# Kernel optimization log

Measured on AMD Instinct MI355X. Metric: run time of the kernel, lower is better.

Reference implementation:

```python
import jax, jax.numpy as jnp
import numpy as np

V, D, H = 50000, 256, 4
HD = H * D            # concat head dim (TransformerConv concat=True)
HH, O = 256, 256      # invariant_hidden_dim, invariant_out_dim
B, N, E, L, A = 16, 1000, 4000, 64, 128
PAD = 0
SCALE = 1.0 / float(np.sqrt(D))


def emb_lookup(table, idx):
    # nn.Embedding with padding_idx: forward is a plain gather; grad at pad row is zeroed.
    rows = table[idx]
    return jnp.where((idx == PAD)[..., None], jax.lax.stop_gradient(rows), rows)


def transformer_conv(x, edge_index, ea, Wq, bq, Wk, bk, Wv, bv, We, Wskip, bskip):
    # PyG TransformerConv, heads=H, concat=True, root_weight=True, beta=False, dropout=0 (eval)
    n = x.shape[0]
    src, dst = edge_index[0], edge_index[1]
    q = (x @ Wq + bq).reshape(n, H, D)
    e = (ea @ We).reshape(-1, H, D)          # lin_edge (bias=False)
    k = (x @ Wk + bk).reshape(n, H, D)[src] + e
    v = (x @ Wv + bv).reshape(n, H, D)[src] + e
    alpha = (q[dst] * k).sum(-1) * SCALE      # [E,H]
    amax = jax.ops.segment_max(alpha, dst, num_segments=n)
    ex = jnp.exp(alpha - amax[dst])
    denom = jax.ops.segment_sum(ex, dst, num_segments=n)
    w = ex / denom[dst]                       # per-target-node softmax over incoming edges
    agg = jax.ops.segment_sum(v * w[..., None], dst, num_segments=n)
    return agg.reshape(n, HD) + x @ Wskip + bskip  # lin_skip on root


def mixed_embed(tok, node, graph_repr, emb):
    fixed = emb_lookup(emb, tok)
    flex = jnp.take_along_axis(graph_repr, node[..., None], axis=1)
    flex = jnp.where((node == PAD)[..., None], jax.lax.stop_gradient(flex), flex)
    return fixed + flex


def gru_last(xs, W_ih, W_hh, b_ih, b_hh):
    # torch nn.GRU, batch_first, 1 layer; only last hidden state is used
    gx = jnp.einsum('blh,gh->blg', xs, W_ih) + b_ih  # [B,L,3O]

    def step(h, g):
        gh = h @ W_hh.T + b_hh
        xr, xz, xn = jnp.split(g, 3, axis=-1)
        hr, hz, hn = jnp.split(gh, 3, axis=-1)
        r = jax.nn.sigmoid(xr + hr)
        z = jax.nn.sigmoid(xz + hz)
        c = jnp.tanh(xn + r * hn)
        return (1.0 - z) * c + z * h, None

    h0 = jnp.zeros((xs.shape[0], W_hh.shape[1]), xs.dtype)
    h_last, _ = jax.lax.scan(step, h0, jnp.swapaxes(gx, 0, 1))
    return h_last


def setup_inputs() -> dict:
    key = jax.random.key(0)
    ks = jax.random.split(key, 40)
    f = lambda i, shape, s=0.05: jax.random.normal(ks[i], shape, jnp.float32) * s
    ri = lambda i, shape, hi: jax.random.randint(ks[i], shape, 0, hi)
    return {
        'node_tokens': ri(0, (B, N), V),
        'edge_tokens': ri(1, (B, E), V),
        'edge_index': ri(2, (B, 2, E), N),
        'inv_token': ri(3, (B, L), V),
        'inv_node': ri(4, (B, L), N),
        'aa_token': ri(5, (B, A), V),
        'aa_node': ri(6, (B, A), N),
        'action_mask': jnp.ones((B, A), jnp.float32),
        'emb': f(7, (V, D), 0.02),
        'Wq': f(8, (D, HD)), 'bq': f(9, (HD,)),
        'Wk': f(10, (D, HD)), 'bk': f(11, (HD,)),
        'Wv': f(12, (D, HD)), 'bv': f(13, (HD,)),
        'We': f(14, (D, HD)),
        'Wskip': f(15, (D, HD)), 'bskip': f(16, (HD,)),
        'W1': f(17, (HD, D)), 'b1': f(18, (D,)),
        'Wp': f(19, (D, HH)), 'bp': f(20, (HH,)),
        'W_ih': f(21, (3 * O, HH)), 'W_hh': f(22, (3 * O, O)),
        'b_ih': f(23, (3 * O,)), 'b_hh': f(24, (3 * O,)),
        'Wab': f(25, (D, 1)), 'bab': f(26, (1,)),
        'Wap': f(27, (D, O)), 'bap': f(28, (O,)),
    }


def reference(node_tokens, edge_tokens, edge_index, inv_token, inv_node, aa_token, aa_node,
              action_mask, emb, Wq, bq, Wk, bk, Wv, bv, We, Wskip, bskip, W1, b1,
              Wp, bp, W_ih, W_hh, b_ih, b_hh, Wab, bab, Wap, bap):
    x = emb_lookup(emb, node_tokens)    # [B,N,D]
    ea = emb_lookup(emb, edge_tokens)   # [B,E,D]
    conv = jax.vmap(lambda xx, ei, ee: transformer_conv(
        xx, ei, ee, Wq, bq, Wk, bk, Wv, bv, We, Wskip, bskip))
    h = jax.nn.relu(conv(x, edge_index, ea))            # [B,N,HD]
    graph_repr = jax.nn.relu(h @ W1 + b1)               # [B,N,D]
    inv_h = jax.nn.relu(mixed_embed(inv_token, inv_node, graph_repr, emb) @ Wp + bp)
    inv = gru_last(inv_h, W_ih, W_hh, b_ih, b_hh)       # [B,O]
    aa_emb = mixed_embed(aa_token, aa_node, graph_repr, emb)  # [B,A,D]
    scores = jnp.einsum('bao,bo->ba', aa_emb @ Wap + bap, inv) + (aa_emb @ Wab + bab)[..., 0]
    inf_mask = jnp.maximum(jnp.log(action_mask), jnp.float32(np.finfo(np.float32).min))
    return scores + inf_mask
```

## Files before the change

kernel.cpp:

```cpp
#include <hip/hip_runtime.h>
#include <hip/hip_bf16.h>
#include <float.h>
#include <math.h>

typedef __hip_bfloat16 bf16;

#define B_ 16
#define N_ 1000
#define E_ 4000
#define L_ 64
#define A_ 128
#define D_ 256
#define H_ 4
#define HD_ 1024
#define SCALE_ 0.0625f

typedef __attribute__((ext_vector_type(8))) short short8;
typedef __attribute__((ext_vector_type(4))) float f32x4;

union U4S8 { uint4 u; short8 s; };

__device__ __forceinline__ unsigned short f2bf(float f) {
    bf16 h = __float2bfloat16(f);
    return *reinterpret_cast<unsigned short*>(&h);
}
__device__ __forceinline__ unsigned pack2(float a, float b) {
    return (unsigned)f2bf(a) | ((unsigned)f2bf(b) << 16);
}
__device__ __forceinline__ float bflo(unsigned u) { return __uint_as_float(u << 16); }
__device__ __forceinline__ float bfhi(unsigned u) { return __uint_as_float(u & 0xffff0000u); }

__global__ void convemb_kernel(const float* __restrict__ src, bf16* __restrict__ dst, long n4)
{
    long i = (long)blockIdx.x * 256 + threadIdx.x;
    if (i >= n4) return;
    float4 v = *(const float4*)(src + i * 4);
    *(uint2*)(dst + i * 4) = make_uint2(pack2(v.x, v.y), pack2(v.z, v.w));
}

__global__ void pack_w_kernel(const float* __restrict__ src, unsigned* __restrict__ dst,
                              int K, int N, int dstN, int colOff, int trans)
{
    int idx = blockIdx.x * 256 + threadIdx.x;
    if (idx >= (K / 2) * N) return;
    int k2 = idx / N, n = idx % N;
    float a, b;
    if (!trans) { a = src[(long)(2 * k2) * N + n]; b = src[(long)(2 * k2 + 1) * N + n]; }
    else        { a = src[(long)n * K + 2 * k2];   b = src[(long)n * K + 2 * k2 + 1]; }
    dst[(long)k2 * dstN + colOff + n] = pack2(a, b);
}

__global__ void bias4_kernel(const float* b0, const float* b1, const float* b2,
                             const float* b3, float* __restrict__ dst)
{
    int i = blockIdx.x * 256 + threadIdx.x;
    if (i >= 4096) return;
    int q = i >> 10, c = i & 1023;
    const float* s = (q == 0) ? b0 : (q == 1) ? b1 : (q == 2) ? b2 : b3;
    dst[i] = s[c];
}

#define TM 128
#define TN 128
#define TK 32
#define ASTR 40
#define BSTR 132

template <typename CT>
__global__ __launch_bounds__(256)
void pgemm_kernel(const bf16* __restrict__ A, const int* __restrict__ arows,
                  const unsigned* __restrict__ Bp, const float* __restrict__ bias,
                  CT* __restrict__ C, int M, int K, int Nc, int relu_out)
{
    __shared__ short    As[TM * ASTR];
    __shared__ unsigned Bs[(TK / 2) * BSTR];

    const int tid  = threadIdx.x;
    const int lane = tid & 63;
    const int wave = tid >> 6;
    const int wm = wave >> 1, wn = wave & 1;
    const int quad = lane >> 4, c16 = lane & 15;
    const long row0 = (long)blockIdx.y * TM;
    const int  col0 = blockIdx.x * TN;

    const int sm  = tid >> 1;
    const int sh  = (tid & 1) * 16;
    const int sn2 = tid & 63;
    const int skk = (tid >> 6) * 4;

    long gr_row = row0 + sm;
    if (gr_row > M - 1) gr_row = M - 1;
    long ar = arows ? (long)arows[gr_row] : gr_row;
    const short* Arow = (const short*)A + ar * K + sh;

    f32x4 acc[4][4];
    #pragma unroll
    for (int i = 0; i < 4; ++i)
        #pragma unroll
        for (int j = 0; j < 4; ++j)
            acc[i][j] = (f32x4){0.f, 0.f, 0.f, 0.f};

    for (int k0 = 0; k0 < K; k0 += TK) {
        {
            const short* p = Arow + k0;
            uint4 a = *(const uint4*)(p);
            uint4 b = *(const uint4*)(p + 8);
            *(uint4*)&As[sm * ASTR + sh]     = a;
            *(uint4*)&As[sm * ASTR + sh + 8] = b;
        }
        #pragma unroll
        for (int i = 0; i < 4; ++i) {
            int kk2 = skk + i;
            *(uint2*)&Bs[kk2 * BSTR + sn2 * 2] =
                *(const uint2*)&Bp[(long)(k0 / 2 + kk2) * Nc + col0 + sn2 * 2];
        }
        __syncthreads();

        short8 af[4];
        U4S8   bfr[4];
        #pragma unroll
        for (int mi = 0; mi < 4; ++mi) {
            int m = wm * 64 + mi * 16 + c16;
            af[mi] = *(const short8*)&As[m * ASTR + quad * 8];
        }
        #pragma unroll
        for (int ni = 0; ni < 4; ++ni) {
            int n = wn * 64 + ni * 16 + c16;
            uint4 u;
            u.x = Bs[(quad * 4 + 0) * BSTR + n];
            u.y = Bs[(quad * 4 + 1) * BSTR + n];
            u.z = Bs[(quad * 4 + 2) * BSTR + n];
            u.w = Bs[(quad * 4 + 3) * BSTR + n];
            bfr[ni].u = u;
        }
        #pragma unroll
        for (int mi = 0; mi < 4; ++mi)
            #pragma unroll
            for (int ni = 0; ni < 4; ++ni)
                acc[mi][ni] = __builtin_amdgcn_mfma_f32_16x16x32_bf16(
                    af[mi], bfr[ni].s, acc[mi][ni], 0, 0, 0);
        __syncthreads();
    }

    #pragma unroll
    for (int ni = 0; ni < 4; ++ni) {
        int col = col0 + wn * 64 + ni * 16 + c16;
        float bv = bias ? bias[col] : 0.f;
        #pragma unroll
        for (int mi = 0; mi < 4; ++mi) {
            long row = row0 + wm * 64 + mi * 16 + quad * 4;
            #pragma unroll
            for (int r = 0; r < 4; ++r) {
                if (row + r >= M) continue;
                float v = acc[mi][ni][r] + bv;
                if (relu_out) v = fmaxf(v, 0.f);
                C[(row + r) * Nc + col] = (CT)v;
            }
        }
    }
}

__global__ void zero_int_kernel(int* __restrict__ p, int n)
{
    int i = blockIdx.x * 256 + threadIdx.x;
    if (i < n) p[i] = 0;
}

__global__ void count_kernel(const int* __restrict__ edge_index, int b0,
                             int* __restrict__ cnt, int cE)
{
    int i = blockIdx.x * 256 + threadIdx.x;
    if (i >= cE) return;
    int bl = i / E_, ei = i % E_;
    int dst = edge_index[(long)(b0 + bl) * 2 * E_ + E_ + ei];
    atomicAdd(&cnt[bl * N_ + dst], 1);
}

__global__ __launch_bounds__(1024)
void scan_kernel(const int* __restrict__ cnt, int* __restrict__ row_start,
                 int* __restrict__ cursor)
{
    int bl = blockIdx.x;
    int tid = threadIdx.x;
    __shared__ int s[1024];
    int v = (tid < N_) ? cnt[bl * N_ + tid] : 0;
    s[tid] = v;
    __syncthreads();
    for (int off = 1; off < 1024; off <<= 1) {
        int t = (tid >= off) ? s[tid - off] : 0;
        __syncthreads();
        s[tid] += t;
        __syncthreads();
    }
    if (tid < N_) {
        int excl = s[tid] - v;
        row_start[bl * N_ + tid] = excl;
        cursor[bl * N_ + tid] = excl;
    }
}

__global__ void scatter_kernel(const int* __restrict__ edge_index, int b0,
                               int* __restrict__ cursor, int* __restrict__ elist, int cE)
{
    int i = blockIdx.x * 256 + threadIdx.x;
    if (i >= cE) return;
    int bl = i / E_, ei = i % E_;
    int dst = edge_index[(long)(b0 + bl) * 2 * E_ + E_ + ei];
    int pos = atomicAdd(&cursor[bl * N_ + dst], 1);
    elist[bl * E_ + pos] = ei;
}

__device__ __forceinline__ float qke2(unsigned q, unsigned k, unsigned e)
{
    return bflo(q) * (bflo(k) + bflo(e)) + bfhi(q) * (bfhi(k) + bfhi(e));
}

__global__ void alpha_ex_kernel(const bf16* __restrict__ qkvs, const bf16* __restrict__ e,
                                const int* __restrict__ edge_index,
                                int b0, float* __restrict__ ex, int cE)
{
    int eidx = blockIdx.x * 4 + (threadIdx.x >> 6);
    int l = threadIdx.x & 63;
    int bl = eidx / E_, ei = eidx % E_;
    const int* eb = edge_index + (long)(b0 + bl) * 2 * E_;
    int src = eb[ei], dst = eb[E_ + ei];
    int head = l >> 4;
    int j0 = head * 256 + (l & 15) * 16;

    const uint4* qp = (const uint4*)(qkvs + (long)(bl * N_ + dst) * 4096 + j0);
    const uint4* kp = (const uint4*)(qkvs + (long)(bl * N_ + src) * 4096 + 1024 + j0);
    const uint4* ep = (const uint4*)(e + (long)eidx * HD_ + j0);

    uint4 qa = qp[0], qb2 = qp[1];
    uint4 ka = kp[0], kb2 = kp[1];
    uint4 ea = ep[0], eb2 = ep[1];

    float s = qke2(qa.x, ka.x, ea.x) + qke2(qa.y, ka.y, ea.y)
            + qke2(qa.z, ka.z, ea.z) + qke2(qa.w, ka.w, ea.w)
            + qke2(qb2.x, kb2.x, eb2.x) + qke2(qb2.y, kb2.y, eb2.y)
            + qke2(qb2.z, kb2.z, eb2.z) + qke2(qb2.w, kb2.w, eb2.w);

    s += __shfl_down(s, 8);
    s += __shfl_down(s, 4);
    s += __shfl_down(s, 2);
    s += __shfl_down(s, 1);

    if ((l & 15) == 0)
        ex[(long)head * cE + eidx] = expf(s * SCALE_);
}

__global__ void agg_node_kernel(const bf16* __restrict__ qkvs, const bf16* __restrict__ e,
                                const float* __restrict__ ex, const int* __restrict__ edge_index,
                                const int* __restrict__ row_start, const int* __restrict__ cnt,
                                const int* __restrict__ elist,
                                int b0, int cE, bf16* __restrict__ aggb)
{
    int base = blockIdx.x;
    int bl = base / N_;
    int tid = threadIdx.x;
    int h = tid >> 6;
    int j0 = tid * 4;

    int start = row_start[base];
    int deg = cnt[base];
    const int* el = elist + (long)bl * E_;
    const float* exh = ex + (long)h * cE;
    const int* srcp = edge_index + (long)(b0 + bl) * 2 * E_;

    float d = 0.f;
    for (int t = 0; t < deg; ++t)
        d += exh[(long)bl * E_ + el[start + t]];
    float invd = (deg > 0) ? 1.f / d : 0.f;

    float a0 = 0.f, a1 = 0.f, a2 = 0.f, a3 = 0.f;
    for (int t = 0; t < deg; ++t) {
        int ei = el[start + t];
        long eidx = (long)bl * E_ + ei;
        float w = exh[eidx] * invd;
        int src = srcp[ei];
        uint2 vv = *(const uint2*)(qkvs + (long)(bl * N_ + src) * 4096 + 2048 + j0);
        uint2 ee = *(const uint2*)(e + eidx * HD_ + j0);
        a0 += w * (bflo(vv.x) + bflo(ee.x));
        a1 += w * (bfhi(vv.x) + bfhi(ee.x));
        a2 += w * (bflo(vv.y) + bflo(ee.y));
        a3 += w * (bfhi(vv.y) + bfhi(ee.y));
    }

    uint2 sk = *(const uint2*)(qkvs + (long)base * 4096 + 3072 + j0);
    unsigned o0 = pack2(fmaxf(bflo(sk.x) + a0, 0.f), fmaxf(bfhi(sk.x) + a1, 0.f));
    unsigned o1 = pack2(fmaxf(bflo(sk.y) + a2, 0.f), fmaxf(bfhi(sk.y) + a3, 0.f));
    *(uint2*)(aggb + (long)base * HD_ + j0) = make_uint2(o0, o1);
}

__global__ void mixed_kernel(const bf16* __restrict__ embh, const int* __restrict__ tok,
                             const int* __restrict__ node, const float* __restrict__ graph_repr,
                             int rows_per_batch, bf16* __restrict__ out)
{
    int r = blockIdx.x;
    int b = r / rows_per_batch;
    int d = threadIdx.x;
    float v = (float)embh[(long)tok[r] * D_ + d] +
              graph_repr[((long)b * N_ + node[r]) * D_ + d];
    out[(long)r * D_ + d] = __float2bfloat16(v);
}

#define GSTR 780

__global__ __launch_bounds__(512, 2)
void gru_kernel(const bf16* __restrict__ gxh, const float* __restrict__ W_hh,
                const float* __restrict__ b_hh, float* __restrict__ inv_out)
{
    __shared__ float gatesLDS[16 * GSTR];
    __shared__ short hB[16 * 264];
    __shared__ short Wlds[8 * 8 * 64 * 8];

    const int tid = threadIdx.x;
    const int lane = tid & 63;
    const int wave = tid >> 6;
    const int quad = lane >> 4, col = lane & 15;

    for (int i = tid; i < 16 * 264; i += 512) hB[i] = 0;

    short8 wfrag[5][8];
    float bhh[6];
    #pragma unroll
    for (int i = 0; i < 5; ++i) {
        int n = (wave * 6 + i) * 16 + col;
        bhh[i] = b_hh[n];
        #pragma unroll
        for (int tk = 0; tk < 8; ++tk) {
            const float* wp = W_hh + (long)n * 256 + tk * 32 + quad * 8;
            float4 w0 = *(const float4*)wp;
            float4 w1 = *(const float4*)(wp + 4);
            U4S8 u;
            u.u = make_uint4(pack2(w0.x, w0.y), pack2(w0.z, w0.w),
                             pack2(w1.x, w1.y), pack2(w1.z, w1.w));
            wfrag[i][tk] = u.s;
        }
    }
    {
        int n = (wave * 6 + 5) * 16 + col;
        bhh[5] = b_hh[n];
        for (int tk = 0; tk < 8; ++tk) {
            const float* wp = W_hh + (long)n * 256 + tk * 32 + quad * 8;
            float4 w0 = *(const float4*)wp;
            float4 w1 = *(const float4*)(wp + 4);
            U4S8 u;
            u.u = make_uint4(pack2(w0.x, w0.y), pack2(w0.z, w0.w),
                             pack2(w1.x, w1.y), pack2(w1.z, w1.w));
            *(short8*)&Wlds[((wave * 8 + tk) * 64 + lane) * 8] = u.s;
        }
    }

    const int em  = tid >> 5;
    const int ei0 = tid & 31;
    float myh[8];
    #pragma unroll
    for (int j = 0; j < 8; ++j) myh[j] = 0.f;

    uint4 gxr[2][3];
    {
        const short* gp = (const short*)gxh + ((long)em * L_ + 0) * 768 + ei0 * 8;
        gxr[0][0] = *(const uint4*)(gp);
        gxr[0][1] = *(const uint4*)(gp + 256);
        gxr[0][2] = *(const uint4*)(gp + 512);
    }
    __syncthreads();

    for (int t = 0; t < L_; ++t) {
        int par = t & 1;
        {
            int nxt = (t + 1 < L_) ? t + 1 : t;
            const short* gp = (const short*)gxh + ((long)em * L_ + nxt) * 768 + ei0 * 8;
            gxr[par ^ 1][0] = *(const uint4*)(gp);
            gxr[par ^ 1][1] = *(const uint4*)(gp + 256);
            gxr[par ^ 1][2] = *(const uint4*)(gp + 512);
        }

        f32x4 acc[6];
        #pragma unroll
        for (int i = 0; i < 6; ++i)
            acc[i] = (f32x4){bhh[i], bhh[i], bhh[i], bhh[i]};
        #pragma unroll
        for (int tk = 0; tk < 8; ++tk) {
            short8 a = *(const short8*)&hB[col * 264 + tk * 32 + quad * 8];
            #pragma unroll
            for (int i = 0; i < 5; ++i)
                acc[i] = __builtin_amdgcn_mfma_f32_16x16x32_bf16(
                    a, wfrag[i][tk], acc[i], 0, 0, 0);
            short8 bl = *(const short8*)&Wlds[((wave * 8 + tk) * 64 + lane) * 8];
            acc[5] = __builtin_amdgcn_mfma_f32_16x16x32_bf16(a, bl, acc[5], 0, 0, 0);
        }
        #pragma unroll
        for (int i = 0; i < 6; ++i) {
            int n = (wave * 6 + i) * 16 + col;
            #pragma unroll
            for (int r = 0; r < 4; ++r)
                gatesLDS[(quad * 4 + r) * GSTR + n] = acc[i][r];
        }
        __syncthreads();

        float gr[8], gz[8], gn[8];
        {
            const float* g = &gatesLDS[em * GSTR + ei0 * 8];
            *(float4*)&gr[0] = *(const float4*)(g);
            *(float4*)&gr[4] = *(const float4*)(g + 4);
            *(float4*)&gz[0] = *(const float4*)(g + 256);
            *(float4*)&gz[4] = *(const float4*)(g + 260);
            *(float4*)&gn[0] = *(const float4*)(g + 512);
            *(float4*)&gn[4] = *(const float4*)(g + 516);
        }
        unsigned short hh[8];
        #pragma unroll
        for (int j = 0; j < 8; ++j) {
            unsigned xr = ((const unsigned*)&gxr[par][0])[j >> 1];
            unsigned xz = ((const unsigned*)&gxr[par][1])[j >> 1];
            unsigned xn = ((const unsigned*)&gxr[par][2])[j >> 1];
            float fxr = (j & 1) ? bfhi(xr) : bflo(xr);
            float fxz = (j & 1) ? bfhi(xz) : bflo(xz);
            float fxn = (j & 1) ? bfhi(xn) : bflo(xn);
            float r = 1.f / (1.f + __expf(-(fxr + gr[j])));
            float z = 1.f / (1.f + __expf(-(fxz + gz[j])));
            float pre = fxn + r * gn[j];
            pre = fminf(fmaxf(pre, -15.f), 15.f);
            float e2 = __expf(-2.f * pre);
            float cc = (1.f - e2) / (1.f + e2);
            float hn = (1.f - z) * cc + z * myh[j];
            myh[j] = hn;
            hh[j] = f2bf(hn);
        }
        *(uint4*)&hB[em * 264 + ei0 * 8] = *(const uint4*)hh;
        __syncthreads();
    }

    float* op = inv_out + (long)em * 256 + ei0 * 8;
    *(float4*)(op)     = make_float4(myh[0], myh[1], myh[2], myh[3]);
    *(float4*)(op + 4) = make_float4(myh[4], myh[5], myh[6], myh[7]);
}

__global__ void score_kernel(const float* __restrict__ aa_p, const bf16* __restrict__ aa_emb,
                             const float* __restrict__ inv, const float* __restrict__ Wab,
                             const float* __restrict__ bab, const float* __restrict__ mask,
                             float* __restrict__ out)
{
    int r = blockIdx.x * 4 + (threadIdx.x >> 6);
    int l = threadIdx.x & 63;
    int b = r / A_;
    float s = 0.f;
    for (int d = l; d < D_; d += 64)
        s += aa_p[(long)r * D_ + d] * inv[(long)b * D_ + d] +
             (float)aa_emb[(long)r * D_ + d] * Wab[d];
    #pragma unroll
    for (int off = 32; off; off >>= 1) s += __shfl_down(s, off);
    if (l == 0) {
        float lm = logf(mask[r]);
        const float MN = -3.4028234663852886e38f;
        if (!(lm >= MN)) lm = MN;
        out[r] = s + bab[0] + lm;
    }
}

static inline size_t align256(size_t x) { return (x + 255) & ~(size_t)255; }

template <typename CT>
static void launch_pgemm(const bf16* A, const int* arows, const unsigned* Bp,
                         const float* bias, CT* C, int M, int K, int Nc, int relu,
                         hipStream_t s)
{
    dim3 grid(Nc / TN, (M + TM - 1) / TM);
    pgemm_kernel<CT><<<grid, 256, 0, s>>>(A, arows, Bp, bias, C, M, K, Nc, relu);
}

static void launch_pack(const float* src, unsigned* dst, int K, int N, int dstN,
                        int colOff, int trans, hipStream_t s)
{
    int tot = (K / 2) * N;
    pack_w_kernel<<<(tot + 255) / 256, 256, 0, s>>>(src, dst, K, N, dstN, colOff, trans);
}

extern "C" void kernel_launch(void* const* d_in, const int* in_sizes, int n_in,
                              void* d_out, int out_size, void* d_ws, size_t ws_size,
                              hipStream_t stream)
{
    const int* node_tokens = (const int*)d_in[0];
    const int* edge_tokens = (const int*)d_in[1];
    const int* edge_index  = (const int*)d_in[2];
    const int* inv_token   = (const int*)d_in[3];
    const int* inv_node    = (const int*)d_in[4];
    const int* aa_token    = (const int*)d_in[5];
    const int* aa_node     = (const int*)d_in[6];
    const float* action_mask = (const float*)d_in[7];
    const float* emb   = (const float*)d_in[8];
    const float* Wq    = (const float*)d_in[9];
    const float* bq    = (const float*)d_in[10];
    const float* Wk    = (const float*)d_in[11];
    const float* bk    = (const float*)d_in[12];
    const float* Wv    = (const float*)d_in[13];
    const float* bv    = (const float*)d_in[14];
    const float* We    = (const float*)d_in[15];
    const float* Wskip = (const float*)d_in[16];
    const float* bskip = (const float*)d_in[17];
    const float* W1    = (const float*)d_in[18];
    const float* b1    = (const float*)d_in[19];
    const float* Wp    = (const float*)d_in[20];
    const float* bp    = (const float*)d_in[21];
    const float* W_ih  = (const float*)d_in[22];
    const float* W_hh  = (const float*)d_in[23];
    const float* b_ih  = (const float*)d_in[24];
    const float* b_hh  = (const float*)d_in[25];
    const float* Wab   = (const float*)d_in[26];
    const float* bab   = (const float*)d_in[27];
    const float* Wap   = (const float*)d_in[28];
    const float* bap   = (const float*)d_in[29];
    (void)in_sizes; (void)n_in; (void)out_size;

    char* base = (char*)d_ws;
    size_t off = 0;
    auto alloc = [&](size_t bytes) -> char* {
        char* p = base + off;
        off = align256(off + bytes);
        return p;
    };

    const long VD = 50000L * 256;
    bf16*  embh       = (bf16*)alloc(VD * 2);
    float* graph_repr = (float*)alloc((size_t)B_ * N_ * D_ * 4);
    bf16*  mixed_inv  = (bf16*)alloc((size_t)B_ * L_ * D_ * 2);
    bf16*  inv_h      = (bf16*)alloc((size_t)B_ * L_ * D_ * 2);
    bf16*  gxh        = (bf16*)alloc((size_t)B_ * L_ * 768 * 2);
    float* inv_out    = (float*)alloc((size_t)B_ * 256 * 4);
    bf16*  aa_emb     = (bf16*)alloc((size_t)B_ * A_ * D_ * 2);
    float* aa_p       = (float*)alloc((size_t)B_ * A_ * 256 * 4);
    unsigned* qkvsP   = (unsigned*)alloc((size_t)128 * 4096 * 4);
    unsigned* WeP     = (unsigned*)alloc((size_t)128 * 1024 * 4);
    unsigned* W1P     = (unsigned*)alloc((size_t)512 * 256 * 4);
    unsigned* WpP     = (unsigned*)alloc((size_t)128 * 256 * 4);
    unsigned* WihP    = (unsigned*)alloc((size_t)128 * 768 * 4);
    unsigned* WapP    = (unsigned*)alloc((size_t)128 * 256 * 4);
    float* bias4096   = (float*)alloc(4096 * 4);
    size_t persist = off;

    int c = 16;
    while (c > 1) {
        size_t cN = (size_t)c * N_, cEs = (size_t)c * E_;
        size_t chunk = align256(cN * 4096 * 2)
                     + align256(cEs * HD_ * 2)
                     + align256(cN * HD_ * 2)
                     + align256(cEs * H_ * 4)
                     + 3 * align256(cN * 4)
                     + align256(cEs * 4);
        if (persist + chunk <= ws_size) break;
        c >>= 1;
    }
    int cN = c * N_, cE = c * E_;

    bf16*  qkvs  = (bf16*)alloc((size_t)cN * 4096 * 2);
    bf16*  ebuf  = (bf16*)alloc((size_t)cE * HD_ * 2);
    bf16*  aggb  = (bf16*)alloc((size_t)cN * HD_ * 2);
    float* ex    = (float*)alloc((size_t)cE * H_ * 4);
    int*   cnt   = (int*)alloc((size_t)cN * 4);
    int*   rstart= (int*)alloc((size_t)cN * 4);
    int*   cursor= (int*)alloc((size_t)cN * 4);
    int*   elist = (int*)alloc((size_t)cE * 4);

    convemb_kernel<<<(int)((VD / 4 + 255) / 256), 256, 0, stream>>>(emb, embh, VD / 4);
    launch_pack(Wq,    qkvsP, 256, 1024, 4096, 0,    0, stream);
    launch_pack(Wk,    qkvsP, 256, 1024, 4096, 1024, 0, stream);
    launch_pack(Wv,    qkvsP, 256, 1024, 4096, 2048, 0, stream);
    launch_pack(Wskip, qkvsP, 256, 1024, 4096, 3072, 0, stream);
    launch_pack(We,    WeP,   256, 1024, 1024, 0,    0, stream);
    launch_pack(W1,    W1P,  1024,  256,  256, 0,    0, stream);
    launch_pack(Wp,    WpP,   256,  256,  256, 0,    0, stream);
    launch_pack(W_ih,  WihP,  256,  768,  768, 0,    1, stream);
    launch_pack(Wap,   WapP,  256,  256,  256, 0,    0, stream);
    bias4_kernel<<<16, 256, 0, stream>>>(bq, bk, bv, bskip, bias4096);

    for (int b0 = 0; b0 < B_; b0 += c) {
        zero_int_kernel<<<(cN + 255) / 256, 256, 0, stream>>>(cnt, cN);
        count_kernel<<<(cE + 255) / 256, 256, 0, stream>>>(edge_index, b0, cnt, cE);
        scan_kernel<<<c, 1024, 0, stream>>>(cnt, rstart, cursor);
        scatter_kernel<<<(cE + 255) / 256, 256, 0, stream>>>(edge_index, b0, cursor,
                                                             elist, cE);
        launch_pgemm<bf16>(embh, node_tokens + (long)b0 * N_, qkvsP, bias4096, qkvs,
                           cN, D_, 4096, 0, stream);
        launch_pgemm<bf16>(embh, edge_tokens + (long)b0 * E_, WeP, nullptr, ebuf,
                           cE, D_, HD_, 0, stream);
        alpha_ex_kernel<<<cE / 4, 256, 0, stream>>>(qkvs, ebuf, edge_index, b0, ex, cE);
        agg_node_kernel<<<cN, 256, 0, stream>>>(qkvs, ebuf, ex, edge_index, rstart, cnt,
                                                elist, b0, cE, aggb);
        launch_pgemm<float>(aggb, nullptr, W1P, b1,
                            graph_repr + (long)b0 * N_ * D_, cN, HD_, D_, 1, stream);
    }

    mixed_kernel<<<B_ * L_, 256, 0, stream>>>(embh, inv_token, inv_node, graph_repr,
                                              L_, mixed_inv);
    launch_pgemm<bf16>(mixed_inv, nullptr, WpP, bp, inv_h, B_ * L_, D_, 256, 1, stream);
    launch_pgemm<bf16>(inv_h, nullptr, WihP, b_ih, gxh, B_ * L_, 256, 768, 0, stream);
    gru_kernel<<<1, 512, 0, stream>>>(gxh, W_hh, b_hh, inv_out);

    mixed_kernel<<<B_ * A_, 256, 0, stream>>>(embh, aa_token, aa_node, graph_repr,
                                              A_, aa_emb);
    launch_pgemm<float>(aa_emb, nullptr, WapP, bap, aa_p, B_ * A_, D_, 256, 0, stream);
    score_kernel<<<(B_ * A_) / 4, 256, 0, stream>>>(aa_p, aa_emb, inv_out, Wab, bab,
                                                    action_mask, (float*)d_out);
}
```

Measured before the change: 942.6 us.

## Run GRU recurrence with 1024 threads and pre-packed W_hh fragments

```diff
diff --git a/kernel.cpp b/kernel.cpp
--- a/kernel.cpp
+++ b/kernel.cpp
@@ -48,6 +48,23 @@
     if (!trans) { a = src[(long)(2 * k2) * N + n]; b = src[(long)(2 * k2 + 1) * N + n]; }
     else        { a = src[(long)n * K + 2 * k2];   b = src[(long)n * K + 2 * k2 + 1]; }
     dst[(long)k2 * dstN + colOff + n] = pack2(a, b);
+}
+
+__global__ void pack_whh_kernel(const float* __restrict__ W_hh, short8* __restrict__ dst)
+{
+    int idx = blockIdx.x * 256 + threadIdx.x;
+    if (idx >= 24576) return;
+    int lane = idx & 63;
+    int tk = (idx >> 6) & 7;
+    int tile = idx >> 9;
+    int n = tile * 16 + (lane & 15);
+    const float* wp = W_hh + (long)n * 256 + tk * 32 + (lane >> 4) * 8;
+    float4 w0 = *(const float4*)wp;
+    float4 w1 = *(const float4*)(wp + 4);
+    U4S8 u;
+    u.u = make_uint4(pack2(w0.x, w0.y), pack2(w0.z, w0.w),
+                     pack2(w1.x, w1.y), pack2(w1.z, w1.w));
+    dst[idx] = u.s;
 }
 
 __global__ void bias4_kernel(const float* b0, const float* b1, const float* b2,
@@ -306,136 +323,92 @@
 
 #define GSTR 780
 
-__global__ __launch_bounds__(512, 2)
-void gru_kernel(const bf16* __restrict__ gxh, const float* __restrict__ W_hh,
+__global__ __launch_bounds__(1024)
+void gru_kernel(const bf16* __restrict__ gxh, const short8* __restrict__ WhhP,
                 const float* __restrict__ b_hh, float* __restrict__ inv_out)
 {
     __shared__ float gatesLDS[16 * GSTR];
     __shared__ short hB[16 * 264];
-    __shared__ short Wlds[8 * 8 * 64 * 8];
 
     const int tid = threadIdx.x;
     const int lane = tid & 63;
     const int wave = tid >> 6;
     const int quad = lane >> 4, col = lane & 15;
 
-    for (int i = tid; i < 16 * 264; i += 512) hB[i] = 0;
-
-    short8 wfrag[5][8];
-    float bhh[6];
+    for (int i = tid; i < 16 * 264; i += 1024) hB[i] = 0;
+
+    short8 wfrag[3][8];
+    float bhh[3];
     #pragma unroll
-    for (int i = 0; i < 5; ++i) {
-        int n = (wave * 6 + i) * 16 + col;
-        bhh[i] = b_hh[n];
-        #pragma unroll
-        for (int tk = 0; tk < 8; ++tk) {
-            const float* wp = W_hh + (long)n * 256 + tk * 32 + quad * 8;
-            float4 w0 = *(const float4*)wp;
-            float4 w1 = *(const float4*)(wp + 4);
-            U4S8 u;
-            u.u = make_uint4(pack2(w0.x, w0.y), pack2(w0.z, w0.w),
-                             pack2(w1.x, w1.y), pack2(w1.z, w1.w));
-            wfrag[i][tk] = u.s;
-        }
-    }
-    {
-        int n = (wave * 6 + 5) * 16 + col;
-        bhh[5] = b_hh[n];
-        for (int tk = 0; tk < 8; ++tk) {
-            const float* wp = W_hh + (long)n * 256 + tk * 32 + quad * 8;
-            float4 w0 = *(const float4*)wp;
-            float4 w1 = *(const float4*)(wp + 4);
-            U4S8 u;
-            u.u = make_uint4(pack2(w0.x, w0.y), pack2(w0.z, w0.w),
-                             pack2(w1.x, w1.y), pack2(w1.z, w1.w));
-            *(short8*)&Wlds[((wave * 8 + tk) * 64 + lane) * 8] = u.s;
-        }
-    }
-
-    const int em  = tid >> 5;
-    const int ei0 = tid & 31;
-    float myh[8];
-    #pragma unroll
-    for (int j = 0; j < 8; ++j) myh[j] = 0.f;
-
-    uint4 gxr[2][3];
-    {
-        const short* gp = (const short*)gxh + ((long)em * L_ + 0) * 768 + ei0 * 8;
-        gxr[0][0] = *(const uint4*)(gp);
-        gxr[0][1] = *(const uint4*)(gp + 256);
-        gxr[0][2] = *(const uint4*)(gp + 512);
-    }
+    for (int i = 0; i < 3; ++i) {
+        int tile = wave * 3 + i;
+        bhh[i] = b_hh[tile * 16 + col];
+        #pragma unroll
+        for (int tk = 0; tk < 8; ++tk)
+            wfrag[i][tk] = WhhP[(tile * 8 + tk) * 64 + lane];
+    }
+
+    const int em = tid >> 6;
+    const int c0 = (tid & 63) * 4;
+    float myh0 = 0.f, myh1 = 0.f, myh2 = 0.f, myh3 = 0.f;
+
     __syncthreads();
 
     for (int t = 0; t < L_; ++t) {
-        int par = t & 1;
-        {
-            int nxt = (t + 1 < L_) ? t + 1 : t;
-            const short* gp = (const short*)gxh + ((long)em * L_ + nxt) * 768 + ei0 * 8;
-            gxr[par ^ 1][0] = *(const uint4*)(gp);
-            gxr[par ^ 1][1] = *(const uint4*)(gp + 256);
-            gxr[par ^ 1][2] = *(const uint4*)(gp + 512);
-        }
-
-        f32x4 acc[6];
-        #pragma unroll
-        for (int i = 0; i < 6; ++i)
-            acc[i] = (f32x4){bhh[i], bhh[i], bhh[i], bhh[i]};
+        const short* gp = (const short*)gxh + ((long)em * L_ + t) * 768 + c0;
+        uint2 xr2 = *(const uint2*)(gp);
+        uint2 xz2 = *(const uint2*)(gp + 256);
+        uint2 xn2 = *(const uint2*)(gp + 512);
+
+        f32x4 acc0 = (f32x4){bhh[0], bhh[0], bhh[0], bhh[0]};
+        f32x4 acc1 = (f32x4){bhh[1], bhh[1], bhh[1], bhh[1]};
+        f32x4 acc2 = (f32x4){bhh[2], bhh[2], bhh[2], bhh[2]};
         #pragma unroll
         for (int tk = 0; tk < 8; ++tk) {
             short8 a = *(const short8*)&hB[col * 264 + tk * 32 + quad * 8];
-            #pragma unroll
-            for (int i = 0; i < 5; ++i)
-                acc[i] = __builtin_amdgcn_mfma_f32_16x16x32_bf16(
-                    a, wfrag[i][tk], acc[i], 0, 0, 0);
-            short8 bl = *(const short8*)&Wlds[((wave * 8 + tk) * 64 + lane) * 8];
-            acc[5] = __builtin_amdgcn_mfma_f32_16x16x32_bf16(a, bl, acc[5], 0, 0, 0);
-        }
-        #pragma unroll
-        for (int i = 0; i < 6; ++i) {
-            int n = (wave * 6 + i) * 16 + col;
-            #pragma unroll
-            for (int r = 0; r < 4; ++r)
-                gatesLDS[(quad * 4 + r) * GSTR + n] = acc[i][r];
+            acc0 = __builtin_amdgcn_mfma_f32_16x16x32_bf16(a, wfrag[0][tk], acc0, 0, 0, 0);
+            acc1 = __builtin_amdgcn_mfma_f32_16x16x32_bf16(a, wfrag[1][tk], acc1, 0, 0, 0);
+            acc2 = __builtin_amdgcn_mfma_f32_16x16x32_bf16(a, wfrag[2][tk], acc2, 0, 0, 0);
+        }
+        #pragma unroll
+        for (int r = 0; r < 4; ++r) {
+            int m = quad * 4 + r;
+            gatesLDS[m * GSTR + (wave * 3 + 0) * 16 + col] = acc0[r];
+            gatesLDS[m * GSTR + (wave * 3 + 1) * 16 + col] = acc1[r];
+            gatesLDS[m * GSTR + (wave * 3 + 2) * 16 + col] = acc2[r];
         }
         __syncthreads();
 
-        float gr[8], gz[8], gn[8];
-        {
-            const float* g = &gatesLDS[em * GSTR + ei0 * 8];
-            *(float4*)&gr[0] = *(const float4*)(g);
-            *(float4*)&gr[4] = *(const float4*)(g + 4);
-            *(float4*)&gz[0] = *(const float4*)(g + 256);
-            *(float4*)&gz[4] = *(const float4*)(g + 260);
-            *(float4*)&gn[0] = *(const float4*)(g + 512);
-            *(float4*)&gn[4] = *(const float4*)(g + 516);
-        }
-        unsigned short hh[8];
-        #pragma unroll
-        for (int j = 0; j < 8; ++j) {
-            unsigned xr = ((const unsigned*)&gxr[par][0])[j >> 1];
-            unsigned xz = ((const unsigned*)&gxr[par][1])[j >> 1];
-            unsigned xn = ((const unsigned*)&gxr[par][2])[j >> 1];
-            float fxr = (j & 1) ? bfhi(xr) : bflo(xr);
-            float fxz = (j & 1) ? bfhi(xz) : bflo(xz);
-            float fxn = (j & 1) ? bfhi(xn) : bflo(xn);
-            float r = 1.f / (1.f + __expf(-(fxr + gr[j])));
-            float z = 1.f / (1.f + __expf(-(fxz + gz[j])));
-            float pre = fxn + r * gn[j];
+        const float* g = &gatesLDS[em * GSTR + c0];
+        float4 grv = *(const float4*)(g);
+        float4 gzv = *(const float4*)(g + 256);
+        float4 gnv = *(const float4*)(g + 512);
+        float gr[4] = {grv.x, grv.y, grv.z, grv.w};
+        float gz[4] = {gzv.x, gzv.y, gzv.z, gzv.w};
+        float gn[4] = {gnv.x, gnv.y, gnv.z, gnv.w};
+        float xr[4] = {bflo(xr2.x), bfhi(xr2.x), bflo(xr2.y), bfhi(xr2.y)};
+        float xz[4] = {bflo(xz2.x), bfhi(xz2.x), bflo(xz2.y), bfhi(xz2.y)};
+        float xn[4] = {bflo(xn2.x), bfhi(xn2.x), bflo(xn2.y), bfhi(xn2.y)};
+        float hn[4];
+        float hold[4] = {myh0, myh1, myh2, myh3};
+        #pragma unroll
+        for (int j = 0; j < 4; ++j) {
+            float r = 1.f / (1.f + __expf(-(xr[j] + gr[j])));
+            float z = 1.f / (1.f + __expf(-(xz[j] + gz[j])));
+            float pre = xn[j] + r * gn[j];
             pre = fminf(fmaxf(pre, -15.f), 15.f);
             float e2 = __expf(-2.f * pre);
             float cc = (1.f - e2) / (1.f + e2);
-            float hn = (1.f - z) * cc + z * myh[j];
-            myh[j] = hn;
-            hh[j] = f2bf(hn);
-        }
-        *(uint4*)&hB[em * 264 + ei0 * 8] = *(const uint4*)hh;
+            hn[j] = (1.f - z) * cc + z * hold[j];
+        }
+        myh0 = hn[0]; myh1 = hn[1]; myh2 = hn[2]; myh3 = hn[3];
+        *(uint2*)&hB[em * 264 + c0] =
+            make_uint2(pack2(hn[0], hn[1]), pack2(hn[2], hn[3]));
         __syncthreads();
     }
 
-    float* op = inv_out + (long)em * 256 + ei0 * 8;
-    *(float4*)(op)     = make_float4(myh[0], myh[1], myh[2], myh[3]);
-    *(float4*)(op + 4) = make_float4(myh[4], myh[5], myh[6], myh[7]);
+    float* op = inv_out + (long)em * 256 + c0;
+    *(float4*)op = make_float4(myh0, myh1, myh2, myh3);
 }
 
 __global__ void score_kernel(const float* __restrict__ aa_p, const bf16* __restrict__ aa_emb,
@@ -537,6 +510,7 @@
     unsigned* WpP     = (unsigned*)alloc((size_t)128 * 256 * 4);
     unsigned* WihP    = (unsigned*)alloc((size_t)128 * 768 * 4);
     unsigned* WapP    = (unsigned*)alloc((size_t)128 * 256 * 4);
+    short8* WhhP      = (short8*)alloc((size_t)24576 * 16);
     float* bias4096   = (float*)alloc(4096 * 4);
     size_t persist = off;
 
@@ -573,6 +547,7 @@
     launch_pack(Wp,    WpP,   256,  256,  256, 0,    0, stream);
     launch_pack(W_ih,  WihP,  256,  768,  768, 0,    1, stream);
     launch_pack(Wap,   WapP,  256,  256,  256, 0,    0, stream);
+    pack_whh_kernel<<<(24576 + 255) / 256, 256, 0, stream>>>(W_hh, WhhP);
     bias4_kernel<<<16, 256, 0, stream>>>(bq, bk, bv, bskip, bias4096);
 
     for (int b0 = 0; b0 < B_; b0 += c) {
@@ -596,7 +571,7 @@
                                               L_, mixed_inv);
     launch_pgemm<bf16>(mixed_inv, nullptr, WpP, bp, inv_h, B_ * L_, D_, 256, 1, stream);
     launch_pgemm<bf16>(inv_h, nullptr, WihP, b_ih, gxh, B_ * L_, 256, 768, 0, stream);
-    gru_kernel<<<1, 512, 0, stream>>>(gxh, W_hh, b_hh, inv_out);
+    gru_kernel<<<1, 1024, 0, stream>>>(gxh, WhhP, b_hh, inv_out);
 
     mixed_kernel<<<B_ * A_, 256, 0, stream>>>(embh, aa_token, aa_node, graph_repr,
                                               A_, aa_emb);
```

After: 954.1 us. About the same (+1.2%).
